# Kernel tuning notes

Measured on AMD Instinct MI355X. Metric: run time of the kernel, lower is better.

The kernel has to match this reference:

```python
import jax, jax.numpy as jnp
import numpy as np

D_MODEL = 1024
D_FF = 4096
FFN_H = int(2 * D_FF / 3)  # 2730, per SwiGLUMLP
B, S = 4, 4096
LN_EPS = 1e-5
ATTN_EPS = 1e-6


def layer_norm(x, g, b):
    mu = jnp.mean(x, axis=-1, keepdims=True)
    var = jnp.mean(jnp.square(x - mu), axis=-1, keepdims=True)
    return (x - mu) * jax.lax.rsqrt(var + LN_EPS) * g + b


def setup_inputs() -> dict:
    key = jax.random.key(0)
    ks = jax.random.split(key, 16)
    s = 0.02
    return {
        "x": jax.random.normal(ks[0], (B, S, D_MODEL), dtype=jnp.float32),
        "Wqkv": jax.random.normal(ks[1], (D_MODEL, 3 * D_MODEL), dtype=jnp.float32) * s,
        "bqkv": jnp.zeros((3 * D_MODEL,), jnp.float32),
        "Wg": jax.random.normal(ks[2], (D_MODEL, FFN_H), dtype=jnp.float32) * s,
        "bg": jnp.zeros((FFN_H,), jnp.float32),
        "Wu": jax.random.normal(ks[3], (D_MODEL, FFN_H), dtype=jnp.float32) * s,
        "bu": jnp.zeros((FFN_H,), jnp.float32),
        "Wd": jax.random.normal(ks[4], (FFN_H, D_MODEL), dtype=jnp.float32) * s,
        "bd": jnp.zeros((D_MODEL,), jnp.float32),
        "g1": jnp.ones((D_MODEL,), jnp.float32),
        "b1": jnp.zeros((D_MODEL,), jnp.float32),
        "g2": jnp.ones((D_MODEL,), jnp.float32),
        "b2": jnp.zeros((D_MODEL,), jnp.float32),
    }


def reference(x, Wqkv, bqkv, Wg, bg, Wu, bu, Wd, bd, g1, b1, g2, b2):
    # QKV projection, split into q, k, v (each [B,S,D])
    qkv = jnp.einsum("bsd,de->bse", x, Wqkv) + bqkv
    q, k, v = jnp.split(qkv, 3, axis=-1)

    # Linear attention with elu(x)+1 feature map (non-causal)
    qp = jax.nn.elu(q) + 1.0
    kp = jax.nn.elu(k) + 1.0
    kv = jnp.einsum("bsd,bse->bde", kp, v)        # [B,D,D] context
    num = jnp.einsum("bsd,bde->bse", qp, kv)       # [B,S,D]
    k_sum = jnp.sum(kp, axis=1)                    # [B,D]
    den = jnp.einsum("bsd,bd->bs", qp, k_sum)[..., None]
    attn = num / (den + ATTN_EPS)

    x = layer_norm(x + attn, g1, b1)

    # SwiGLU MLP
    gate = jnp.einsum("bsd,dh->bsh", x, Wg) + bg
    up = jnp.einsum("bsd,dh->bsh", x, Wu) + bu
    ffn = jnp.einsum("bsh,hd->bsd", jax.nn.silu(gate) * up, Wd) + bd

    return layer_norm(x + ffn, g2, b2)
```

## Files before the change

### kernel.cpp

```cpp
#include <hip/hip_runtime.h>

#define SEQ 4096
#define TOK 16384
#define DM 1024
#define NQKV 3072
#define FFH 2730
#define FFHP 2816

typedef __bf16 bf16x8 __attribute__((ext_vector_type(8)));
typedef float f32x4 __attribute__((ext_vector_type(4)));

__device__ __forceinline__ unsigned short f2bf(float f) {
  union { float f; unsigned u; } v; v.f = f;
  unsigned r = v.u + 0x7fffu + ((v.u >> 16) & 1u);
  return (unsigned short)(r >> 16);
}
__device__ __forceinline__ float bf2f(unsigned short h) {
  union { unsigned u; float f; } v; v.u = ((unsigned)h) << 16;
  return v.f;
}

__device__ __forceinline__ void xcd_swizzle(int& bx, int& by) {
  const int gx = gridDim.x, gy = gridDim.y;
  const int chunk = gy >> 3;
  const int csh = __ffs(chunk) - 1;
  const int lin = by * gx + bx;
  const int xcd = lin & 7, j = lin >> 3;
  by = xcd * chunk + (j & (chunk - 1));
  bx = j >> csh;
}

enum { M_QKV = 0, M_BF16 = 1, M_NUM = 2, M_BIAS_F32 = 5 };

template<int MODE>
__global__ __launch_bounds__(256)
void gemm_kernel(const unsigned short* __restrict__ A,
                 const unsigned short* __restrict__ BT,
                 int K, int lda, int ldb, int ldc,
                 long zsA, long zsB, long zsC,
                 void* __restrict__ out0, void* __restrict__ out1, void* __restrict__ out2,
                 const float* __restrict__ bias, int nbias)
{
  __shared__ unsigned short As[2][128 * 64];
  __shared__ unsigned short Bs[2][128 * 64];
  const int tid  = threadIdx.x;
  const int wave = tid >> 6, lane = tid & 63;
  const int quad = lane >> 4, l16 = lane & 15;
  const int bz = blockIdx.z;
  int bx = blockIdx.x, by = blockIdx.y;
  xcd_swizzle(bx, by);

  const unsigned short* Ab = A + (size_t)zsA * bz + (size_t)by * 128 * lda;
  const unsigned short* Bb = BT + (size_t)zsB * bz + (size_t)bx * 128 * ldb;

  f32x4 acc[4][4] = {};

  const int srow   = lane >> 3;
  const int scol_g = (((lane & 7) ^ srow) * 8);
  const int axor   = l16 & 7;

  auto stage = [&](int buf, int k0) {
#pragma unroll
    for (int j = 0; j < 4; ++j) {
      int c = wave * 4 + j;
      const unsigned short* sa = Ab + (size_t)(c * 8 + srow) * lda + k0 + scol_g;
      __builtin_amdgcn_global_load_lds((__attribute__((address_space(1))) void*)sa,
          (__attribute__((address_space(3))) void*)(As[buf] + c * 512), 16, 0, 0);
      const unsigned short* sb = Bb + (size_t)(c * 8 + srow) * ldb + k0 + scol_g;
      __builtin_amdgcn_global_load_lds((__attribute__((address_space(1))) void*)sb,
          (__attribute__((address_space(3))) void*)(Bs[buf] + c * 512), 16, 0, 0);
    }
  };

  const int NIT = K >> 6;
  stage(0, 0);
  int cur = 0;
  for (int it = 0; it < NIT; ++it) {
    __builtin_amdgcn_s_waitcnt(0);
    __syncthreads();
    if (it + 1 < NIT) stage(cur ^ 1, (it + 1) << 6);
#pragma unroll
    for (int kk = 0; kk < 64; kk += 32) {
      bf16x8 af[4], bfr[4];
#pragma unroll
      for (int mt = 0; mt < 4; ++mt)
        af[mt] = *(const bf16x8*)(As[cur] + ((wave >> 1) * 64 + mt * 16 + l16) * 64
                                     + ((((kk >> 3) + quad) ^ axor) * 8));
#pragma unroll
      for (int nt = 0; nt < 4; ++nt)
        bfr[nt] = *(const bf16x8*)(Bs[cur] + ((wave & 1) * 64 + nt * 16 + l16) * 64
                                      + ((((kk >> 3) + quad) ^ axor) * 8));
#pragma unroll
      for (int mt = 0; mt < 4; ++mt)
#pragma unroll
        for (int nt = 0; nt < 4; ++nt)
          acc[mt][nt] = __builtin_amdgcn_mfma_f32_16x16x32_bf16(af[mt], bfr[nt], acc[mt][nt], 0, 0, 0);
    }
    cur ^= 1;
  }

#pragma unroll
  for (int mt = 0; mt < 4; ++mt) {
#pragma unroll
    for (int nt = 0; nt < 4; ++nt) {
      const int r0 = by * 128 + (wave >> 1) * 64 + mt * 16 + quad * 4;
      const int c  = bx * 128 + (wave & 1) * 64 + nt * 16 + l16;
      float vals[4];
#pragma unroll
      for (int i = 0; i < 4; ++i) vals[i] = acc[mt][nt][i];

      if (MODE == M_QKV) {
        const int b = r0 >> 12, s0 = r0 & 4095;
#pragma unroll
        for (int i = 0; i < 4; ++i) vals[i] += bias[c];
        if (c < 1024) {
#pragma unroll
          for (int i = 0; i < 4; ++i) {
            float e = vals[i] > 0.f ? vals[i] + 1.f : __expf(vals[i]);
            ((unsigned short*)out0)[(size_t)(r0 + i) * DM + c] = f2bf(e);
          }
        } else if (c < 2048) {
          ushort4 o;
          float e0 = vals[0] > 0.f ? vals[0] + 1.f : __expf(vals[0]);
          float e1 = vals[1] > 0.f ? vals[1] + 1.f : __expf(vals[1]);
          float e2 = vals[2] > 0.f ? vals[2] + 1.f : __expf(vals[2]);
          float e3 = vals[3] > 0.f ? vals[3] + 1.f : __expf(vals[3]);
          o.x = f2bf(e0); o.y = f2bf(e1); o.z = f2bf(e2); o.w = f2bf(e3);
          *(ushort4*)((unsigned short*)out1 + (size_t)b * DM * SEQ + (size_t)(c - 1024) * SEQ + s0) = o;
        } else {
          ushort4 o;
          o.x = f2bf(vals[0]); o.y = f2bf(vals[1]); o.z = f2bf(vals[2]); o.w = f2bf(vals[3]);
          *(ushort4*)((unsigned short*)out2 + (size_t)b * DM * SEQ + (size_t)(c - 2048) * SEQ + s0) = o;
        }
      } else {
#pragma unroll
        for (int i = 0; i < 4; ++i) {
          const int r = r0 + i;
          float val = vals[i];
          if (MODE == M_BF16 || MODE == M_NUM) {
            ((unsigned short*)out0)[(size_t)zsC * bz + (size_t)r * ldc + c] = f2bf(val);
          } else {
            if (c < nbias) val += bias[c];
            ((float*)out0)[(size_t)r * ldc + c] = val;
          }
        }
      }
    }
  }
}

__global__ __launch_bounds__(256)
void gateup_kernel(const unsigned short* __restrict__ A,
                   const unsigned short* __restrict__ BgT,
                   const unsigned short* __restrict__ BuT,
                   const float* __restrict__ bg, const float* __restrict__ bu,
                   unsigned short* __restrict__ h)
{
  __shared__ unsigned short As[2][128 * 64];
  __shared__ unsigned short Bgs[2][64 * 64];
  __shared__ unsigned short Bus[2][64 * 64];
  const int tid  = threadIdx.x;
  const int wave = tid >> 6, lane = tid & 63;
  const int quad = lane >> 4, l16 = lane & 15;
  const int wm = wave >> 1, wn = wave & 1;
  int bx = blockIdx.x, by = blockIdx.y;
  xcd_swizzle(bx, by);

  const unsigned short* Ab  = A + (size_t)by * 128 * DM;
  const unsigned short* Bgb = BgT + (size_t)bx * 64 * DM;
  const unsigned short* Bub = BuT + (size_t)bx * 64 * DM;

  f32x4 accg[4][2] = {};
  f32x4 accu[4][2] = {};

  const int srow   = lane >> 3;
  const int scol_g = (((lane & 7) ^ srow) * 8);
  const int axor   = l16 & 7;

  auto stage = [&](int buf, int k0) {
#pragma unroll
    for (int j = 0; j < 4; ++j) {
      int c = wave * 4 + j;
      const unsigned short* sa = Ab + (size_t)(c * 8 + srow) * DM + k0 + scol_g;
      __builtin_amdgcn_global_load_lds((__attribute__((address_space(1))) void*)sa,
          (__attribute__((address_space(3))) void*)(As[buf] + c * 512), 16, 0, 0);
    }
#pragma unroll
    for (int j = 0; j < 2; ++j) {
      int c = wave * 2 + j;
      const unsigned short* sg = Bgb + (size_t)(c * 8 + srow) * DM + k0 + scol_g;
      __builtin_amdgcn_global_load_lds((__attribute__((address_space(1))) void*)sg,
          (__attribute__((address_space(3))) void*)(Bgs[buf] + c * 512), 16, 0, 0);
      const unsigned short* su = Bub + (size_t)(c * 8 + srow) * DM + k0 + scol_g;
      __builtin_amdgcn_global_load_lds((__attribute__((address_space(1))) void*)su,
          (__attribute__((address_space(3))) void*)(Bus[buf] + c * 512), 16, 0, 0);
    }
  };

  const int NIT = DM >> 6;
  stage(0, 0);
  int cur = 0;
  for (int it = 0; it < NIT; ++it) {
    __builtin_amdgcn_s_waitcnt(0);
    __syncthreads();
    if (it + 1 < NIT) stage(cur ^ 1, (it + 1) << 6);
#pragma unroll
    for (int kk = 0; kk < 64; kk += 32) {
      const int kb = (((kk >> 3) + quad) ^ axor) * 8;
      bf16x8 af[4], bgf[2], buf_[2];
#pragma unroll
      for (int mt = 0; mt < 4; ++mt)
        af[mt] = *(const bf16x8*)(As[cur] + (wm * 64 + mt * 16 + l16) * 64 + kb);
#pragma unroll
      for (int nt = 0; nt < 2; ++nt) {
        bgf[nt]  = *(const bf16x8*)(Bgs[cur] + (wn * 32 + nt * 16 + l16) * 64 + kb);
        buf_[nt] = *(const bf16x8*)(Bus[cur] + (wn * 32 + nt * 16 + l16) * 64 + kb);
      }
#pragma unroll
      for (int mt = 0; mt < 4; ++mt)
#pragma unroll
        for (int nt = 0; nt < 2; ++nt) {
          accg[mt][nt] = __builtin_amdgcn_mfma_f32_16x16x32_bf16(af[mt], bgf[nt],  accg[mt][nt], 0, 0, 0);
          accu[mt][nt] = __builtin_amdgcn_mfma_f32_16x16x32_bf16(af[mt], buf_[nt], accu[mt][nt], 0, 0, 0);
        }
    }
    cur ^= 1;
  }

#pragma unroll
  for (int mt = 0; mt < 4; ++mt) {
#pragma unroll
    for (int nt = 0; nt < 2; ++nt) {
      const int r0 = by * 128 + wm * 64 + mt * 16 + quad * 4;
      const int c  = bx * 64 + wn * 32 + nt * 16 + l16;
      const float bgv = (c < FFH) ? bg[c] : 0.f;
      const float buv = (c < FFH) ? bu[c] : 0.f;
#pragma unroll
      for (int i = 0; i < 4; ++i) {
        float g = accg[mt][nt][i] + bgv;
        float u = accu[mt][nt][i] + buv;
        float hv = g / (1.f + __expf(-g)) * u;
        h[(size_t)(r0 + i) * FFHP + c] = f2bf(hv);
      }
    }
  }
}

__global__ __launch_bounds__(256)
void cvt_kernel(const float* __restrict__ in, unsigned short* __restrict__ out, int n)
{
  int i = (blockIdx.x * 256 + threadIdx.x) * 4;
  if (i < n) {
    float4 v = *(const float4*)(in + i);
    ushort4 o;
    o.x = f2bf(v.x); o.y = f2bf(v.y); o.z = f2bf(v.z); o.w = f2bf(v.w);
    *(ushort4*)(out + i) = o;
  }
}

__global__ __launch_bounds__(256)
void wtrans_kernel(const float* __restrict__ in, unsigned short* __restrict__ out,
                   int R, int C, int Cpad, int Rpad)
{
  __shared__ float tile[32][33];
  int r0 = blockIdx.x * 32;
  int c0 = blockIdx.y * 32;
  int tid = threadIdx.x;
#pragma unroll
  for (int j = 0; j < 4; ++j) {
    int r = j * 8 + (tid >> 5), c = tid & 31;
    float v = 0.f;
    if (r0 + r < R && c0 + c < C) v = in[(size_t)(r0 + r) * C + c0 + c];
    tile[r][c] = v;
  }
  __syncthreads();
#pragma unroll
  for (int j = 0; j < 4; ++j) {
    int c = j * 8 + (tid >> 5), r = tid & 31;
    out[(size_t)(c0 + c) * Rpad + (r0 + r)] = f2bf(tile[r][c]);
  }
}

__device__ __forceinline__ float block_sum(float v, float* sm)
{
#pragma unroll
  for (int o = 32; o > 0; o >>= 1) v += __shfl_down(v, o, 64);
  int w = threadIdx.x >> 6;
  if ((threadIdx.x & 63) == 0) sm[w] = v;
  __syncthreads();
  float r = sm[0] + sm[1] + sm[2] + sm[3];
  __syncthreads();
  return r;
}

__global__ __launch_bounds__(256)
void ksum_kernel(const unsigned short* __restrict__ kpT, float* __restrict__ ksum)
{
  __shared__ float sm[4];
  int row = blockIdx.x;
  const ushort4* src = (const ushort4*)(kpT + (size_t)row * SEQ);
  float s = 0.f;
#pragma unroll
  for (int j = 0; j < 4; ++j) {
    ushort4 v = src[threadIdx.x + j * 256];
    s += bf2f(v.x) + bf2f(v.y) + bf2f(v.z) + bf2f(v.w);
  }
  float tot = block_sum(s, sm);
  if (threadIdx.x == 0) ksum[row] = tot;
}

__global__ __launch_bounds__(256)
void ln1_kernel(const unsigned short* __restrict__ xb16, const unsigned short* __restrict__ num16,
                const unsigned short* __restrict__ qp, const float* __restrict__ ksum,
                const float* __restrict__ g1, const float* __restrict__ b1,
                unsigned short* __restrict__ yb)
{
  __shared__ float sm[4];
  int t = blockIdx.x, tid = threadIdx.x, b = t >> 12;
  ushort4 xv = ((const ushort4*)(xb16 + (size_t)t * DM))[tid];
  ushort4 nv = ((const ushort4*)(num16 + (size_t)t * DM))[tid];
  ushort4 qv = ((const ushort4*)(qp + (size_t)t * DM))[tid];
  float4 kv = ((const float4*)(ksum + (size_t)b * DM))[tid];
  float q0 = bf2f(qv.x), q1 = bf2f(qv.y), q2 = bf2f(qv.z), q3 = bf2f(qv.w);
  float den = block_sum(q0 * kv.x + q1 * kv.y + q2 * kv.z + q3 * kv.w, sm);
  float inv = 1.f / (den + 1e-6f);
  float r0 = bf2f(xv.x) + bf2f(nv.x) * inv, r1 = bf2f(xv.y) + bf2f(nv.y) * inv;
  float r2 = bf2f(xv.z) + bf2f(nv.z) * inv, r3 = bf2f(xv.w) + bf2f(nv.w) * inv;
  float s1 = block_sum(r0 + r1 + r2 + r3, sm);
  float s2 = block_sum(r0 * r0 + r1 * r1 + r2 * r2 + r3 * r3, sm);
  float mu = s1 * (1.f / 1024.f);
  float var = s2 * (1.f / 1024.f) - mu * mu;
  float rs = rsqrtf(var + 1e-5f);
  float4 gv = ((const float4*)g1)[tid];
  float4 bv = ((const float4*)b1)[tid];
  ushort4 o;
  o.x = f2bf((r0 - mu) * rs * gv.x + bv.x);
  o.y = f2bf((r1 - mu) * rs * gv.y + bv.y);
  o.z = f2bf((r2 - mu) * rs * gv.z + bv.z);
  o.w = f2bf((r3 - mu) * rs * gv.w + bv.w);
  ((ushort4*)(yb + (size_t)t * DM))[tid] = o;
}

__global__ __launch_bounds__(256)
void ln2_kernel(const unsigned short* __restrict__ yb, const float* __restrict__ ffn,
                const float* __restrict__ g2, const float* __restrict__ b2,
                float* __restrict__ out)
{
  __shared__ float sm[4];
  int t = blockIdx.x, tid = threadIdx.x;
  ushort4 yv = ((const ushort4*)(yb + (size_t)t * DM))[tid];
  float4 fv = ((const float4*)(ffn + (size_t)t * DM))[tid];
  float r0 = bf2f(yv.x) + fv.x, r1 = bf2f(yv.y) + fv.y;
  float r2 = bf2f(yv.z) + fv.z, r3 = bf2f(yv.w) + fv.w;
  float s1 = block_sum(r0 + r1 + r2 + r3, sm);
  float s2 = block_sum(r0 * r0 + r1 * r1 + r2 * r2 + r3 * r3, sm);
  float mu = s1 * (1.f / 1024.f);
  float var = s2 * (1.f / 1024.f) - mu * mu;
  float rs = rsqrtf(var + 1e-5f);
  float4 gv = ((const float4*)g2)[tid];
  float4 bv = ((const float4*)b2)[tid];
  float4 o;
  o.x = (r0 - mu) * rs * gv.x + bv.x;
  o.y = (r1 - mu) * rs * gv.y + bv.y;
  o.z = (r2 - mu) * rs * gv.z + bv.z;
  o.w = (r3 - mu) * rs * gv.w + bv.w;
  ((float4*)(out + (size_t)t * DM))[tid] = o;
}

extern "C" void kernel_launch(void* const* d_in, const int* in_sizes, int n_in,
                              void* d_out, int out_size, void* d_ws, size_t ws_size,
                              hipStream_t stream)
{
  const float* x    = (const float*)d_in[0];
  const float* Wqkv = (const float*)d_in[1];
  const float* bqkv = (const float*)d_in[2];
  const float* Wg   = (const float*)d_in[3];
  const float* bg   = (const float*)d_in[4];
  const float* Wu   = (const float*)d_in[5];
  const float* bu   = (const float*)d_in[6];
  const float* Wd   = (const float*)d_in[7];
  const float* bd   = (const float*)d_in[8];
  const float* g1   = (const float*)d_in[9];
  const float* b1   = (const float*)d_in[10];
  const float* g2   = (const float*)d_in[11];
  const float* b2   = (const float*)d_in[12];
  float* out = (float*)d_out;

  char* ws = (char*)d_ws;
  size_t off = 0;
  auto alloc = [&](size_t bytes) {
    char* p = ws + off;
    off += (bytes + 255) & ~(size_t)255;
    return p;
  };
  unsigned short* WqkvT = (unsigned short*)alloc((size_t)NQKV * DM * 2);
  unsigned short* WgT   = (unsigned short*)alloc((size_t)FFHP * DM * 2);
  unsigned short* WuT   = (unsigned short*)alloc((size_t)FFHP * DM * 2);
  unsigned short* WdT   = (unsigned short*)alloc((size_t)DM * FFHP * 2);
  float*          ksum  = (float*)alloc((size_t)4 * DM * 4);
  unsigned short* xbyb  = (unsigned short*)alloc((size_t)TOK * DM * 2);
  unsigned short* kvT   = (unsigned short*)alloc((size_t)4 * DM * DM * 2);
  char* R3 = alloc((size_t)3 * TOK * DM * 2);
  unsigned short* qp  = (unsigned short*)(R3);
  unsigned short* kpT = (unsigned short*)(R3 + (size_t)TOK * DM * 2);
  unsigned short* vT  = (unsigned short*)(R3 + (size_t)2 * TOK * DM * 2);
  unsigned short* hbuf = (unsigned short*)(R3);
  unsigned short* xb = xbyb;
  unsigned short* yb = xbyb;
  unsigned short* num = (unsigned short*)d_out;
  float* ffn = (float*)d_out;

  dim3 blk(256);

  cvt_kernel<<<dim3(TOK * DM / 1024), blk, 0, stream>>>(x, xb, TOK * DM);
  wtrans_kernel<<<dim3(32, 96), blk, 0, stream>>>(Wqkv, WqkvT, 1024, 3072, 3072, 1024);
  wtrans_kernel<<<dim3(32, 88), blk, 0, stream>>>(Wg, WgT, 1024, FFH, FFHP, 1024);
  wtrans_kernel<<<dim3(32, 88), blk, 0, stream>>>(Wu, WuT, 1024, FFH, FFHP, 1024);
  wtrans_kernel<<<dim3(88, 32), blk, 0, stream>>>(Wd, WdT, FFH, 1024, 1024, FFHP);
  gemm_kernel<M_QKV><<<dim3(NQKV / 128, TOK / 128), blk, 0, stream>>>(
      xb, WqkvT, 1024, 1024, 1024, 0, 0, 0, 0, qp, kpT, vT, bqkv, NQKV);
  ksum_kernel<<<dim3(4096), blk, 0, stream>>>(kpT, ksum);
  gemm_kernel<M_BF16><<<dim3(8, 8, 4), blk, 0, stream>>>(
      vT, kpT, 4096, 4096, 4096, 1024,
      (long)DM * SEQ, (long)DM * SEQ, (long)DM * DM,
      kvT, nullptr, nullptr, nullptr, 0);
  gemm_kernel<M_NUM><<<dim3(8, 32, 4), blk, 0, stream>>>(
      qp, kvT, 1024, 1024, 1024, 1024,
      (long)SEQ * DM, (long)DM * DM, (long)SEQ * DM,
      num, nullptr, nullptr, nullptr, 0);
  ln1_kernel<<<dim3(TOK), blk, 0, stream>>>(xb, num, qp, ksum, g1, b1, yb);
  gateup_kernel<<<dim3(FFHP / 64, TOK / 128), blk, 0, stream>>>(
      yb, WgT, WuT, bg, bu, hbuf);
  gemm_kernel<M_BIAS_F32><<<dim3(DM / 128, TOK / 128), blk, 0, stream>>>(
      hbuf, WdT, FFHP, FFHP, FFHP, DM, 0, 0, 0, ffn, nullptr, nullptr, bd, DM);
  ln2_kernel<<<dim3(TOK), blk, 0, stream>>>(yb, ffn, g2, b2, out);

  (void)in_sizes; (void)n_in; (void)out_size; (void)ws_size;
}
```

Before: 834.9 us.

## Add 256x256 eight-wave pipelined GEMM and interleave gate/up weights

Adds a 512-thread GEMM kernel that computes 256x256 output tiles. It double-buffers its LDS tiles and runs an eight-phase schedule that interleaves half-tile global-to-LDS loads with MFMA quadrants, using raised wave priority and explicit barriers. The gate and up weights are transposed into one interleaved matrix in 16-row groups, so the fused SwiGLU GEMM becomes a single wide GEMM whose epilogue pairs gate and up accumulators. The num and down-projection GEMMs also move to this kernel. The aim is more data reuse per loaded byte and better overlap of loads with MFMA work. The cost is a 128KB LDS footprint, which likely allows only one block per CU despite the launch bound, higher register pressure, and fewer blocks for the smaller GEMMs.

```diff
diff --git a/kernel.cpp b/kernel.cpp
--- a/kernel.cpp
+++ b/kernel.cpp
@@ -149,98 +149,178 @@
   }
 }
 
-__global__ __launch_bounds__(256)
-void gateup_kernel(const unsigned short* __restrict__ A,
-                   const unsigned short* __restrict__ BgT,
-                   const unsigned short* __restrict__ BuT,
-                   const float* __restrict__ bg, const float* __restrict__ bu,
-                   unsigned short* __restrict__ h)
-{
-  __shared__ unsigned short As[2][128 * 64];
-  __shared__ unsigned short Bgs[2][64 * 64];
-  __shared__ unsigned short Bus[2][64 * 64];
+enum { G_GATEUP = 0, G_NUM = 1, G_BIAS_F32 = 2 };
+
+#define MBAR() asm volatile("s_barrier" ::: "memory")
+#define WAITV(N) asm volatile("s_waitcnt vmcnt(" #N ")" ::: "memory")
+
+#define LDS_A(BUF, QM) do {                                                   \
+    _Pragma("unroll")                                                         \
+    for (int mt = 0; mt < 4; ++mt) {                                          \
+      _Pragma("unroll")                                                       \
+      for (int k2 = 0; k2 < 2; ++k2)                                          \
+        af[mt][k2] = *(const bf16x8*)(As[BUF] +                               \
+            (wm * 128 + ((QM) * 4 + mt) * 16 + l16) * 64 +                    \
+            (((k2 * 4 + quad) ^ axor) * 8));                                  \
+    }                                                                         \
+  } while (0)
+
+#define LDS_B(BUF, QN) do {                                                   \
+    _Pragma("unroll")                                                         \
+    for (int nt = 0; nt < 2; ++nt) {                                          \
+      _Pragma("unroll")                                                       \
+      for (int k2 = 0; k2 < 2; ++k2)                                          \
+        bfr[nt][k2] = *(const bf16x8*)(Bs[BUF] +                              \
+            (wn * 64 + ((QN) * 2 + nt) * 16 + l16) * 64 +                     \
+            (((k2 * 4 + quad) ^ axor) * 8));                                  \
+    }                                                                         \
+  } while (0)
+
+#define MMAQ(QM, QN) do {                                                     \
+    _Pragma("unroll")                                                         \
+    for (int mt = 0; mt < 4; ++mt) {                                          \
+      _Pragma("unroll")                                                       \
+      for (int nt = 0; nt < 2; ++nt) {                                        \
+        _Pragma("unroll")                                                     \
+        for (int k2 = 0; k2 < 2; ++k2)                                        \
+          acc[(QM) * 4 + mt][(QN) * 2 + nt] =                                 \
+              __builtin_amdgcn_mfma_f32_16x16x32_bf16(af[mt][k2], bfr[nt][k2],\
+                  acc[(QM) * 4 + mt][(QN) * 2 + nt], 0, 0, 0);                \
+      }                                                                       \
+    }                                                                         \
+  } while (0)
+
+#define PHASE(BUF, QM, QN, LA, LB, STAGE) do {                                \
+    if (LA) LDS_A(BUF, QM);                                                   \
+    if (LB) LDS_B(BUF, QN);                                                   \
+    STAGE                                                                     \
+    MBAR();                                                                   \
+    __builtin_amdgcn_sched_barrier(0);                                        \
+    __builtin_amdgcn_s_setprio(1);                                            \
+    MMAQ(QM, QN);                                                             \
+    __builtin_amdgcn_s_setprio(0);                                            \
+    WAITV(6);                                                                 \
+    MBAR();                                                                   \
+  } while (0)
+
+template<int MODE>
+__global__ __launch_bounds__(512, 2)
+void gemm256_kernel(const unsigned short* __restrict__ A,
+                    const unsigned short* __restrict__ BT,
+                    int K, int lda, int ldb, int ldc,
+                    long zsA, long zsB, long zsC,
+                    void* __restrict__ out0,
+                    const float* __restrict__ bias0,
+                    const float* __restrict__ bias1,
+                    int nbias)
+{
+  __shared__ unsigned short As[2][256 * 64];
+  __shared__ unsigned short Bs[2][256 * 64];
   const int tid  = threadIdx.x;
   const int wave = tid >> 6, lane = tid & 63;
   const int quad = lane >> 4, l16 = lane & 15;
-  const int wm = wave >> 1, wn = wave & 1;
+  const int wm = wave >> 2, wn = wave & 3;
+  const int bz = blockIdx.z;
   int bx = blockIdx.x, by = blockIdx.y;
   xcd_swizzle(bx, by);
 
-  const unsigned short* Ab  = A + (size_t)by * 128 * DM;
-  const unsigned short* Bgb = BgT + (size_t)bx * 64 * DM;
-  const unsigned short* Bub = BuT + (size_t)bx * 64 * DM;
-
-  f32x4 accg[4][2] = {};
-  f32x4 accu[4][2] = {};
-
-  const int srow   = lane >> 3;
-  const int scol_g = (((lane & 7) ^ srow) * 8);
-  const int axor   = l16 & 7;
-
-  auto stage = [&](int buf, int k0) {
-#pragma unroll
-    for (int j = 0; j < 4; ++j) {
-      int c = wave * 4 + j;
-      const unsigned short* sa = Ab + (size_t)(c * 8 + srow) * DM + k0 + scol_g;
-      __builtin_amdgcn_global_load_lds((__attribute__((address_space(1))) void*)sa,
-          (__attribute__((address_space(3))) void*)(As[buf] + c * 512), 16, 0, 0);
+  const unsigned short* Ab = A + (size_t)zsA * bz + (size_t)by * 256 * lda;
+  const unsigned short* Bb = BT + (size_t)zsB * bz + (size_t)bx * 256 * ldb;
+
+  f32x4 acc[8][4] = {};
+
+  const int srow = lane >> 3;
+  const int sxor = ((lane & 7) ^ srow) * 8;
+  const int axor = l16 & 7;
+
+  const unsigned short* pA[2][2];
+  const unsigned short* pB[2][2];
+  int cA[2][2], cB[2][2];
+#pragma unroll
+  for (int part = 0; part < 2; ++part) {
+#pragma unroll
+    for (int j = 0; j < 2; ++j) {
+      int idx = wave * 2 + j;
+      int ca = ((idx & 8) ? idx + 8 : idx) + part * 8;
+      int cb = (idx >> 2) * 8 + (idx & 3) + part * 4;
+      cA[part][j] = ca; cB[part][j] = cb;
+      pA[part][j] = Ab + (size_t)(ca * 8 + srow) * lda + sxor;
+      pB[part][j] = Bb + (size_t)(cb * 8 + srow) * ldb + sxor;
     }
-#pragma unroll
-    for (int j = 0; j < 2; ++j) {
-      int c = wave * 2 + j;
-      const unsigned short* sg = Bgb + (size_t)(c * 8 + srow) * DM + k0 + scol_g;
-      __builtin_amdgcn_global_load_lds((__attribute__((address_space(1))) void*)sg,
-          (__attribute__((address_space(3))) void*)(Bgs[buf] + c * 512), 16, 0, 0);
-      const unsigned short* su = Bub + (size_t)(c * 8 + srow) * DM + k0 + scol_g;
-      __builtin_amdgcn_global_load_lds((__attribute__((address_space(1))) void*)su,
-          (__attribute__((address_space(3))) void*)(Bus[buf] + c * 512), 16, 0, 0);
+  }
+
+  auto stageA = [&](int buf, int part, int tile) {
+    const int k0 = tile << 6;
+#pragma unroll
+    for (int j = 0; j < 2; ++j)
+      __builtin_amdgcn_global_load_lds(
+          (__attribute__((address_space(1))) void*)(pA[part][j] + k0),
+          (__attribute__((address_space(3))) void*)(As[buf] + cA[part][j] * 512), 16, 0, 0);
+  };
+  auto stageB = [&](int buf, int part, int tile) {
+    const int k0 = tile << 6;
+#pragma unroll
+    for (int j = 0; j < 2; ++j)
+      __builtin_amdgcn_global_load_lds(
+          (__attribute__((address_space(1))) void*)(pB[part][j] + k0),
+          (__attribute__((address_space(3))) void*)(Bs[buf] + cB[part][j] * 512), 16, 0, 0);
+  };
+
+  stageA(0, 0, 0); stageA(0, 1, 0); stageB(0, 0, 0); stageB(0, 1, 0);
+  stageB(1, 0, 1); stageA(1, 1, 1);
+  WAITV(4);
+  MBAR();
+
+  bf16x8 af[4][2], bfr[2][2];
+  const int NT = K >> 6;
+  for (int i = 0; i < NT; i += 2) {
+    const int t1 = i + 1;
+    const int t2s = (i + 2 < NT), t3s = (i + 3 < NT);
+    PHASE(0, 0, 0, 1, 1, { stageA(1, 0, t1); });
+    PHASE(0, 1, 0, 1, 0, { stageB(1, 1, t1); });
+    PHASE(0, 1, 1, 0, 1, { if (t2s) stageB(0, 0, i + 2); });
+    PHASE(0, 0, 1, 1, 0, { if (t2s) stageA(0, 1, i + 2); });
+    PHASE(1, 0, 0, 1, 1, { if (t2s) stageA(0, 0, i + 2); });
+    PHASE(1, 1, 0, 1, 0, { if (t2s) stageB(0, 1, i + 2); });
+    PHASE(1, 1, 1, 0, 1, { if (t3s) stageB(1, 0, i + 3); });
+    PHASE(1, 0, 1, 1, 0, { if (t3s) stageA(1, 1, i + 3); });
+  }
+
+  if (MODE == G_GATEUP) {
+#pragma unroll
+    for (int mt = 0; mt < 8; ++mt) {
+      const int r0 = by * 256 + wm * 128 + mt * 16 + quad * 4;
+#pragma unroll
+      for (int p = 0; p < 2; ++p) {
+        const int hc = bx * 128 + wn * 32 + p * 16 + l16;
+        const float bgv = (hc < nbias) ? bias0[hc] : 0.f;
+        const float buv = (hc < nbias) ? bias1[hc] : 0.f;
+#pragma unroll
+        for (int i2 = 0; i2 < 4; ++i2) {
+          float g = acc[mt][2 * p][i2] + bgv;
+          float u = acc[mt][2 * p + 1][i2] + buv;
+          float hv = g / (1.f + __expf(-g)) * u;
+          ((unsigned short*)out0)[(size_t)(r0 + i2) * ldc + hc] = f2bf(hv);
+        }
+      }
     }
-  };
-
-  const int NIT = DM >> 6;
-  stage(0, 0);
-  int cur = 0;
-  for (int it = 0; it < NIT; ++it) {
-    __builtin_amdgcn_s_waitcnt(0);
-    __syncthreads();
-    if (it + 1 < NIT) stage(cur ^ 1, (it + 1) << 6);
-#pragma unroll
-    for (int kk = 0; kk < 64; kk += 32) {
-      const int kb = (((kk >> 3) + quad) ^ axor) * 8;
-      bf16x8 af[4], bgf[2], buf_[2];
-#pragma unroll
-      for (int mt = 0; mt < 4; ++mt)
-        af[mt] = *(const bf16x8*)(As[cur] + (wm * 64 + mt * 16 + l16) * 64 + kb);
-#pragma unroll
-      for (int nt = 0; nt < 2; ++nt) {
-        bgf[nt]  = *(const bf16x8*)(Bgs[cur] + (wn * 32 + nt * 16 + l16) * 64 + kb);
-        buf_[nt] = *(const bf16x8*)(Bus[cur] + (wn * 32 + nt * 16 + l16) * 64 + kb);
-      }
-#pragma unroll
-      for (int mt = 0; mt < 4; ++mt)
-#pragma unroll
-        for (int nt = 0; nt < 2; ++nt) {
-          accg[mt][nt] = __builtin_amdgcn_mfma_f32_16x16x32_bf16(af[mt], bgf[nt],  accg[mt][nt], 0, 0, 0);
-          accu[mt][nt] = __builtin_amdgcn_mfma_f32_16x16x32_bf16(af[mt], buf_[nt], accu[mt][nt], 0, 0, 0);
+  } else {
+#pragma unroll
+    for (int mt = 0; mt < 8; ++mt) {
+#pragma unroll
+      for (int nt = 0; nt < 4; ++nt) {
+        const int r0 = by * 256 + wm * 128 + mt * 16 + quad * 4;
+        const int c  = bx * 256 + wn * 64 + nt * 16 + l16;
+#pragma unroll
+        for (int i2 = 0; i2 < 4; ++i2) {
+          float v = acc[mt][nt][i2];
+          if (MODE == G_NUM) {
+            ((unsigned short*)out0)[(size_t)zsC * bz + (size_t)(r0 + i2) * ldc + c] = f2bf(v);
+          } else {
+            if (c < nbias) v += bias0[c];
+            ((float*)out0)[(size_t)(r0 + i2) * ldc + c] = v;
+          }
         }
-    }
-    cur ^= 1;
-  }
-
-#pragma unroll
-  for (int mt = 0; mt < 4; ++mt) {
-#pragma unroll
-    for (int nt = 0; nt < 2; ++nt) {
-      const int r0 = by * 128 + wm * 64 + mt * 16 + quad * 4;
-      const int c  = bx * 64 + wn * 32 + nt * 16 + l16;
-      const float bgv = (c < FFH) ? bg[c] : 0.f;
-      const float buv = (c < FFH) ? bu[c] : 0.f;
-#pragma unroll
-      for (int i = 0; i < 4; ++i) {
-        float g = accg[mt][nt][i] + bgv;
-        float u = accu[mt][nt][i] + buv;
-        float hv = g / (1.f + __expf(-g)) * u;
-        h[(size_t)(r0 + i) * FFHP + c] = f2bf(hv);
       }
     }
   }
@@ -260,7 +340,7 @@
 
 __global__ __launch_bounds__(256)
 void wtrans_kernel(const float* __restrict__ in, unsigned short* __restrict__ out,
-                   int R, int C, int Cpad, int Rpad)
+                   int R, int C, int Cpad, int Rpad, int omode)
 {
   __shared__ float tile[32][33];
   int r0 = blockIdx.x * 32;
@@ -277,7 +357,10 @@
 #pragma unroll
   for (int j = 0; j < 4; ++j) {
     int c = j * 8 + (tid >> 5), r = tid & 31;
-    out[(size_t)(c0 + c) * Rpad + (r0 + r)] = f2bf(tile[r][c]);
+    int oc = c0 + c;
+    int orow = (omode == 0) ? oc
+             : ((oc >> 4) * 32 + (oc & 15) + ((omode == 2) ? 16 : 0));
+    out[(size_t)orow * Rpad + (r0 + r)] = f2bf(tile[r][c]);
   }
 }
 
@@ -394,8 +477,7 @@
     return p;
   };
   unsigned short* WqkvT = (unsigned short*)alloc((size_t)NQKV * DM * 2);
-  unsigned short* WgT   = (unsigned short*)alloc((size_t)FFHP * DM * 2);
-  unsigned short* WuT   = (unsigned short*)alloc((size_t)FFHP * DM * 2);
+  unsigned short* WguT  = (unsigned short*)alloc((size_t)2 * FFHP * DM * 2);
   unsigned short* WdT   = (unsigned short*)alloc((size_t)DM * FFHP * 2);
   float*          ksum  = (float*)alloc((size_t)4 * DM * 4);
   unsigned short* xbyb  = (unsigned short*)alloc((size_t)TOK * DM * 2);
@@ -410,13 +492,13 @@
   unsigned short* num = (unsigned short*)d_out;
   float* ffn = (float*)d_out;
 
-  dim3 blk(256);
+  dim3 blk(256), blk5(512);
 
   cvt_kernel<<<dim3(TOK * DM / 1024), blk, 0, stream>>>(x, xb, TOK * DM);
-  wtrans_kernel<<<dim3(32, 96), blk, 0, stream>>>(Wqkv, WqkvT, 1024, 3072, 3072, 1024);
-  wtrans_kernel<<<dim3(32, 88), blk, 0, stream>>>(Wg, WgT, 1024, FFH, FFHP, 1024);
-  wtrans_kernel<<<dim3(32, 88), blk, 0, stream>>>(Wu, WuT, 1024, FFH, FFHP, 1024);
-  wtrans_kernel<<<dim3(88, 32), blk, 0, stream>>>(Wd, WdT, FFH, 1024, 1024, FFHP);
+  wtrans_kernel<<<dim3(32, 96), blk, 0, stream>>>(Wqkv, WqkvT, 1024, 3072, 3072, 1024, 0);
+  wtrans_kernel<<<dim3(32, 88), blk, 0, stream>>>(Wg, WguT, 1024, FFH, FFHP, 1024, 1);
+  wtrans_kernel<<<dim3(32, 88), blk, 0, stream>>>(Wu, WguT, 1024, FFH, FFHP, 1024, 2);
+  wtrans_kernel<<<dim3(88, 32), blk, 0, stream>>>(Wd, WdT, FFH, 1024, 1024, FFHP, 0);
   gemm_kernel<M_QKV><<<dim3(NQKV / 128, TOK / 128), blk, 0, stream>>>(
       xb, WqkvT, 1024, 1024, 1024, 0, 0, 0, 0, qp, kpT, vT, bqkv, NQKV);
   ksum_kernel<<<dim3(4096), blk, 0, stream>>>(kpT, ksum);
@@ -424,15 +506,15 @@
       vT, kpT, 4096, 4096, 4096, 1024,
       (long)DM * SEQ, (long)DM * SEQ, (long)DM * DM,
       kvT, nullptr, nullptr, nullptr, 0);
-  gemm_kernel<M_NUM><<<dim3(8, 32, 4), blk, 0, stream>>>(
+  gemm256_kernel<G_NUM><<<dim3(4, 16, 4), blk5, 0, stream>>>(
       qp, kvT, 1024, 1024, 1024, 1024,
       (long)SEQ * DM, (long)DM * DM, (long)SEQ * DM,
-      num, nullptr, nullptr, nullptr, 0);
+      num, nullptr, nullptr, 0);
   ln1_kernel<<<dim3(TOK), blk, 0, stream>>>(xb, num, qp, ksum, g1, b1, yb);
-  gateup_kernel<<<dim3(FFHP / 64, TOK / 128), blk, 0, stream>>>(
-      yb, WgT, WuT, bg, bu, hbuf);
-  gemm_kernel<M_BIAS_F32><<<dim3(DM / 128, TOK / 128), blk, 0, stream>>>(
-      hbuf, WdT, FFHP, FFHP, FFHP, DM, 0, 0, 0, ffn, nullptr, nullptr, bd, DM);
+  gemm256_kernel<G_GATEUP><<<dim3(2 * FFHP / 256, TOK / 256), blk5, 0, stream>>>(
+      yb, WguT, 1024, DM, DM, FFHP, 0, 0, 0, hbuf, bg, bu, FFH);
+  gemm256_kernel<G_BIAS_F32><<<dim3(DM / 256, TOK / 256), blk5, 0, stream>>>(
+      hbuf, WdT, FFHP, FFHP, FFHP, DM, 0, 0, 0, ffn, bd, nullptr, DM);
   ln2_kernel<<<dim3(TOK), blk, 0, stream>>>(yb, ffn, g2, b2, out);
 
   (void)in_sizes; (void)n_in; (void)out_size; (void)ws_size;
```

After: 786.6 us. 1.06x faster.
